# Kernel optimization log

Measured on AMD Instinct MI355X. Metric: run time of the kernel, lower is better.

## Reference

```python
import jax, jax.numpy as jnp
import numpy as np

S, B, V, E, H, T = 256, 32, 50000, 300, 256, 32  # seq, batch, vocab, emb, lstm hidden, num_tags


def _lstm_dir(x, w_ih, w_hh, b_ih, b_hh, reverse):
    # x: [S, B, in]; gates in PyTorch order i, f, g, o
    Bm, Hm = x.shape[1], w_hh.shape[1]
    def step(carry, xt):
        h, c = carry
        g = xt @ w_ih.T + b_ih + h @ w_hh.T + b_hh  # [B, 4H]
        i, f, gg, o = jnp.split(g, 4, axis=-1)
        c = jax.nn.sigmoid(f) * c + jax.nn.sigmoid(i) * jnp.tanh(gg)
        h = jax.nn.sigmoid(o) * jnp.tanh(c)
        return (h, c), h
    init = (jnp.zeros((Bm, Hm), x.dtype), jnp.zeros((Bm, Hm), x.dtype))
    _, hs = jax.lax.scan(step, init, x, reverse=reverse)
    return hs  # [S, B, H]


def _crf_loss(em, tags, start, trans, end):
    # em: [S, B, T]; torchcrf log-likelihood, reduction='sum', full mask
    bidx = jnp.arange(em.shape[1])
    # numerator (gold path score)
    emit = jnp.take_along_axis(em, tags[:, :, None], axis=2)[..., 0].sum(0)  # [B]
    tr = trans[tags[:-1], tags[1:]].sum(0)  # [B]
    num = start[tags[0]] + emit + tr + end[tags[-1]]
    # denominator (forward algorithm)
    def step(alpha, e):
        alpha = jax.nn.logsumexp(alpha[:, :, None] + trans[None] + e[:, None, :], axis=1)
        return alpha, None
    alpha0 = start[None] + em[0]  # [B, T]
    alpha, _ = jax.lax.scan(step, alpha0, em[1:])
    logZ = jax.nn.logsumexp(alpha + end[None], axis=-1)  # [B]
    return -(num - logZ).sum()


def _viterbi(em, start, trans, end):
    def step(s, e):
        cand = s[:, :, None] + trans[None]           # [B, T_prev, T_cur]
        return cand.max(1) + e, cand.argmax(1)        # score [B,T], backptr [B,T]
    score0 = start[None] + em[0]
    score, hist = jax.lax.scan(step, score0, em[1:])  # hist: [S-1, B, T]
    last = jnp.argmax(score + end[None], axis=-1)     # [B]
    def back(tag, bp):
        prev = jnp.take_along_axis(bp, tag[:, None], axis=1)[:, 0]
        return prev, prev
    _, path_head = jax.lax.scan(back, last, hist, reverse=True)  # [S-1, B]
    return jnp.concatenate([path_head, last[None]], axis=0).astype(jnp.int32)  # [S, B]


def setup_inputs():
    key = jax.random.key(0)
    ks = jax.random.split(key, 32)
    def n(k, shape, s=0.1):
        return (jax.random.normal(k, shape, jnp.float32) * s)
    inp = {
        'words': jax.random.randint(ks[0], (S, B), 0, V),
        'chars': jax.random.randint(ks[1], (S, B, 16), 0, 100),
        'tags': jax.random.randint(ks[2], (S, B), 0, T),
        'emb_table': n(ks[3], (V, E)),
        'fc_w': n(ks[4], (T, 2 * H), float(np.sqrt(2.0 / (T + 2 * H)))),
        'fc_b': n(ks[5], (T,), float(np.sqrt(1.0 / T))),
        'crf_start': n(ks[6], (T,)),
        'crf_end': n(ks[7], (T,)),
        'crf_trans': n(ks[8], (T, T)),
    }
    i = 9
    for l, din in ((0, E), (1, 2 * H)):
        for d in ('f', 'b'):
            inp[f'w_ih_l{l}{d}'] = n(ks[i], (4 * H, din)); i += 1
            inp[f'w_hh_l{l}{d}'] = n(ks[i], (4 * H, H)); i += 1
            inp[f'b_ih_l{l}{d}'] = n(ks[i], (4 * H,)); i += 1
            inp[f'b_hh_l{l}{d}'] = n(ks[i], (4 * H,)); i += 1
    return inp


def reference(words, chars, tags, emb_table, fc_w, fc_b, crf_start, crf_end, crf_trans,
              w_ih_l0f, w_hh_l0f, b_ih_l0f, b_hh_l0f,
              w_ih_l0b, w_hh_l0b, b_ih_l0b, b_hh_l0b,
              w_ih_l1f, w_hh_l1f, b_ih_l1f, b_hh_l1f,
              w_ih_l1b, w_hh_l1b, b_ih_l1b, b_hh_l1b):
    # chars / char CNN are unused in the original forward()
    x = emb_table[words]                                   # [S, B, E]
    h0 = jnp.concatenate([
        _lstm_dir(x, w_ih_l0f, w_hh_l0f, b_ih_l0f, b_hh_l0f, False),
        _lstm_dir(x, w_ih_l0b, w_hh_l0b, b_ih_l0b, b_hh_l0b, True)], axis=-1)
    h1 = jnp.concatenate([
        _lstm_dir(h0, w_ih_l1f, w_hh_l1f, b_ih_l1f, b_hh_l1f, False),
        _lstm_dir(h0, w_ih_l1b, w_hh_l1b, b_ih_l1b, b_hh_l1b, True)], axis=-1)  # [S, B, 2H]
    em = h1 @ fc_w.T + fc_b                                # emissions [S, B, T]
    crf_out = _viterbi(em, crf_start, crf_trans, crf_end)  # [S, B] int32
    crf_loss = _crf_loss(em, tags, crf_start, crf_trans, crf_end)
    return crf_out, crf_loss
```

## Files before the change

kernel.cpp:

```cpp
#include <hip/hip_runtime.h>
#include <stdint.h>

#define S_ 256
#define B_ 32
#define H_ 256
#define G4_ 1024
#define HXW (16*132)

typedef short bf16x8 __attribute__((ext_vector_type(8)));
typedef float f32x4  __attribute__((ext_vector_type(4)));

__device__ __forceinline__ unsigned f2bf(float f){
  unsigned u = __float_as_uint(f);
  return (u + 0x7fffu + ((u >> 16) & 1u)) >> 16;
}
__device__ __forceinline__ float bfl(unsigned u){ return __uint_as_float(u << 16); }
__device__ __forceinline__ float bfh(unsigned u){ return __uint_as_float(u & 0xffff0000u); }
__device__ __forceinline__ float sigf(float x){ return 1.0f / (1.0f + __expf(-x)); }
__device__ __forceinline__ float thf(float x){
  x = fminf(fmaxf(x, -15.0f), 15.0f);
  float e = __expf(2.0f * x);
  return (e - 1.0f) / (e + 1.0f);
}

__device__ __forceinline__ int hval_ok(unsigned long long v){
  return (((unsigned)v & (unsigned)(v >> 32)) & 0x40004000u) == 0x40004000u;
}

__global__ __launch_bounds__(320) void k_prep(const int* __restrict__ words,
                                              const float* __restrict__ emb,
                                              unsigned short* __restrict__ x,
                                              unsigned* __restrict__ hbuf0){
  int row = blockIdx.x;
  int e = threadIdx.x;
  int w = words[row];
  x[row * 320 + e] = (e < 300) ? (unsigned short)f2bf(emb[w * 300 + e]) : 0;
  if (e < 256) hbuf0[row * 256 + e] = 0;
}

__global__ __launch_bounds__(256) void k_packw(
    const float* __restrict__ w0f, const float* __restrict__ w0b,
    const float* __restrict__ w1f, const float* __restrict__ w1b,
    const float* __restrict__ fw,
    unsigned short* __restrict__ wb0f, unsigned short* __restrict__ wb0b,
    unsigned short* __restrict__ wb1f, unsigned short* __restrict__ wb1b,
    unsigned short* __restrict__ fcwb){
  int r = blockIdx.x, tid = threadIdx.x;
  if (r < 2048){
    int rr = r & 1023;
    const float* src = (r < 1024) ? w0f : w0b;
    unsigned short* dst = (r < 1024) ? wb0f : wb0b;
    for (int e = tid; e < 320; e += 256)
      dst[rr * 320 + e] = (e < 300) ? (unsigned short)f2bf(src[rr * 300 + e]) : 0;
  } else if (r < 4096){
    int rr = r & 1023;
    const float* src = (r < 3072) ? w1f : w1b;
    unsigned short* dst = (r < 3072) ? wb1f : wb1b;
    for (int e = tid; e < 512; e += 256)
      dst[rr * 512 + e] = (unsigned short)f2bf(src[rr * 512 + e]);
  } else {
    int rr = r - 4096;
    for (int e = tid; e < 512; e += 256)
      fcwb[rr * 512 + e] = (unsigned short)f2bf(fw[rr * 512 + e]);
  }
}

__global__ __launch_bounds__(256) void k_gemm_bf2(
    const unsigned short* __restrict__ A, int lda, int nSteps,
    const unsigned short* __restrict__ Bf, const unsigned short* __restrict__ Bb,
    const float* __restrict__ b1f, const float* __restrict__ b2f,
    const float* __restrict__ b1b, const float* __restrict__ b2b,
    float* __restrict__ Cf, float* __restrict__ Cb){
  const int z = blockIdx.z;
  const unsigned short* __restrict__ B = z ? Bb : Bf;
  const float* __restrict__ bias1 = z ? b1b : b1f;
  const float* __restrict__ bias2 = z ? b2b : b2f;
  float* __restrict__ C = z ? Cb : Cf;

  __shared__ __align__(16) unsigned As[64 * 20];
  __shared__ __align__(16) unsigned Bs[128 * 20];
  const int tid = threadIdx.x;
  const int w = tid >> 6, lane = tid & 63;
  const int quad = lane >> 4, coln = lane & 15;
  const int m0 = blockIdx.y * 64, n0 = blockIdx.x * 128;

  f32x4 acc[8];
  #pragma unroll
  for (int i = 0; i < 8; ++i){ acc[i][0]=0.f; acc[i][1]=0.f; acc[i][2]=0.f; acc[i][3]=0.f; }

  for (int kt = 0; kt < nSteps; ++kt){
    int k0 = kt * 32;
    __syncthreads();
    {
      int row = tid >> 2, part = tid & 3;
      *(uint4*)&As[row * 20 + part * 4] =
          *(const uint4*)(A + (size_t)(m0 + row) * lda + k0 + part * 8);
    }
    #pragma unroll
    for (int i = 0; i < 2; ++i){
      int idx = tid + 256 * i;
      int row = idx >> 2, part = idx & 3;
      *(uint4*)&Bs[row * 20 + part * 4] =
          *(const uint4*)(B + (size_t)(n0 + row) * lda + k0 + part * 8);
    }
    __syncthreads();
    union { uint4 q; bf16x8 v; } au;
    au.q = *(const uint4*)&As[(w * 16 + coln) * 20 + quad * 4];
    #pragma unroll
    for (int nt = 0; nt < 8; ++nt){
      union { uint4 q; bf16x8 v; } bu;
      bu.q = *(const uint4*)&Bs[(nt * 16 + coln) * 20 + quad * 4];
      acc[nt] = __builtin_amdgcn_mfma_f32_16x16x32_bf16(au.v, bu.v, acc[nt], 0, 0, 0);
    }
  }
  #pragma unroll
  for (int nt = 0; nt < 8; ++nt){
    int col = n0 + nt * 16 + coln;
    float bs = bias1[col] + bias2[col];
    #pragma unroll
    for (int reg = 0; reg < 4; ++reg)
      C[(size_t)(m0 + w * 16 + quad * 4 + reg) * 1024 + col] = acc[nt][reg] + bs;
  }
}

__global__ __launch_bounds__(256, 1) void k_lstm2(
    const float* __restrict__ Gf, const float* __restrict__ Gb,
    const float* __restrict__ Whf, const float* __restrict__ Whb,
    unsigned* __restrict__ hbuf,
    unsigned short* __restrict__ Hout)
{
  __shared__ __align__(16) unsigned hx[2 * HXW];
  const int wg  = blockIdx.x;
  const int dir = wg >> 3, n = (wg >> 1) & 3, bh = wg & 1;
  const float* __restrict__ G  = dir ? Gb : Gf;
  const float* __restrict__ Wh = dir ? Whb : Whf;
  const int tid  = threadIdx.x;
  const int w    = tid >> 6;
  const int lane = tid & 63;
  const int quad = lane >> 4, coln = lane & 15;

  bf16x8 Wr[32];
  #pragma unroll
  for (int ks = 0; ks < 8; ++ks){
    #pragma unroll
    for (int gt = 0; gt < 4; ++gt){
      const float* wp = Wh + (size_t)(gt * 256 + (n << 6) + (w << 4) + coln) * 256
                        + ks * 32 + quad * 8;
      float4 a = *(const float4*)wp;
      float4 b = *(const float4*)(wp + 4);
      union { unsigned u[4]; bf16x8 v; } tu;
      tu.u[0] = f2bf(a.x) | (f2bf(a.y) << 16);
      tu.u[1] = f2bf(a.z) | (f2bf(a.w) << 16);
      tu.u[2] = f2bf(b.x) | (f2bf(b.y) << 16);
      tu.u[3] = f2bf(b.z) | (f2bf(b.w) << 16);
      Wr[ks * 4 + gt] = tu.v;
    }
  }

  const int gu  = (n << 6) + (w << 4) + coln;
  const int mrw = quad << 2;

  float c0 = 0.f, c1 = 0.f, c2 = 0.f, c3 = 0.f;

  for (int t = 0; t < 256; ++t){
    int s = dir ? (255 - t) : t;
    f32x4 acc[4];
    #pragma unroll
    for (int gt = 0; gt < 4; ++gt){
      const float* gp = G + (size_t)(s * 32 + bh * 16 + mrw) * 1024 + gt * 256 + gu;
      f32x4 a;
      a[0] = gp[0]; a[1] = gp[1024]; a[2] = gp[2048]; a[3] = gp[3072];
      acc[gt] = a;
    }
    unsigned* hxr = &hx[(t & 1) * HXW];
    if (t > 0){
      const unsigned* hb = hbuf + (((size_t)(t - 1) * 2 + dir) * 2 + bh) * 2048;
      int row = tid >> 4, kk = tid & 15;
      int n1 = (n + 1) & 3, n2 = (n + 2) & 3, n3 = (n + 3) & 3;
      const unsigned long long* p1 =
          (const unsigned long long*)(hb + row * 128 + n1 * 32 + kk * 2);
      const unsigned long long* p2 =
          (const unsigned long long*)(hb + row * 128 + n2 * 32 + kk * 2);
      const unsigned long long* p3 =
          (const unsigned long long*)(hb + row * 128 + n3 * 32 + kk * 2);
      unsigned long long v1, v2, v3;
      do {
        v1 = __hip_atomic_load(p1, __ATOMIC_RELAXED, __HIP_MEMORY_SCOPE_AGENT);
        v2 = __hip_atomic_load(p2, __ATOMIC_RELAXED, __HIP_MEMORY_SCOPE_AGENT);
        v3 = __hip_atomic_load(p3, __ATOMIC_RELAXED, __HIP_MEMORY_SCOPE_AGENT);
      } while (!(hval_ok(v1) && hval_ok(v2) && hval_ok(v3)));
      hxr[row * 132 + n1 * 32 + kk * 2]     = (unsigned)v1 & 0xBFFFBFFFu;
      hxr[row * 132 + n1 * 32 + kk * 2 + 1] = (unsigned)(v1 >> 32) & 0xBFFFBFFFu;
      hxr[row * 132 + n2 * 32 + kk * 2]     = (unsigned)v2 & 0xBFFFBFFFu;
      hxr[row * 132 + n2 * 32 + kk * 2 + 1] = (unsigned)(v2 >> 32) & 0xBFFFBFFFu;
      hxr[row * 132 + n3 * 32 + kk * 2]     = (unsigned)v3 & 0xBFFFBFFFu;
      hxr[row * 132 + n3 * 32 + kk * 2 + 1] = (unsigned)(v3 >> 32) & 0xBFFFBFFFu;
      __syncthreads();
      #pragma unroll
      for (int ks = 0; ks < 8; ++ks){
        union { uint4 q; bf16x8 v; } tu;
        tu.q = *(const uint4*)&hxr[coln * 132 + ks * 16 + quad * 4];
        #pragma unroll
        for (int gt = 0; gt < 4; ++gt)
          acc[gt] = __builtin_amdgcn_mfma_f32_16x16x32_bf16(tu.v, Wr[ks * 4 + gt],
                                                            acc[gt], 0, 0, 0);
      }
    }
    unsigned* hxw = &hx[((t + 1) & 1) * HXW];
    unsigned* hw  = hbuf + (((size_t)t * 2 + dir) * 2 + bh) * 2048;
    float cc[4] = {c0, c1, c2, c3};
    #pragma unroll
    for (int reg = 0; reg < 4; ++reg){
      float gi = sigf(acc[0][reg]);
      float gf = sigf(acc[1][reg]);
      float gg = thf (acc[2][reg]);
      float go = sigf(acc[3][reg]);
      float cv = gf * cc[reg] + gi * gg;
      cc[reg] = cv;
      float hv = go * thf(cv);
      unsigned hb16 = f2bf(hv);
      unsigned other = (unsigned)__shfl_xor((int)hb16, 1);
      if (!(coln & 1)){
        unsigned pair = hb16 | (other << 16);
        hxw[(mrw + reg) * 132 + (gu >> 1)] = pair;
        if (t < 255)
          __hip_atomic_store(hw + (mrw + reg) * 128 + (gu >> 1),
                             pair | 0x40004000u,
                             __ATOMIC_RELAXED, __HIP_MEMORY_SCOPE_AGENT);
      }
      Hout[(size_t)(s * 32 + bh * 16 + mrw + reg) * 512 + dir * 256 + gu] =
          (unsigned short)hb16;
    }
    c0 = cc[0]; c1 = cc[1]; c2 = cc[2]; c3 = cc[3];
  }
}

__global__ __launch_bounds__(64) void k_fc(const unsigned short* __restrict__ h1,
                                           const unsigned short* __restrict__ fw,
                                           const float* __restrict__ fb,
                                           float* __restrict__ em){
  int row = blockIdx.x;
  int lane = threadIdx.x;
  int tag = lane & 31, half = lane >> 5;
  const uint4* hp = (const uint4*)(h1 + (size_t)row * 512 + half * 256);
  const uint4* wp = (const uint4*)(fw + (size_t)tag * 512 + half * 256);
  float acc = 0.0f;
  #pragma unroll 8
  for (int i = 0; i < 32; ++i){
    uint4 h = hp[i], v = wp[i];
    acc += bfl(h.x) * bfl(v.x) + bfh(h.x) * bfh(v.x)
         + bfl(h.y) * bfl(v.y) + bfh(h.y) * bfh(v.y)
         + bfl(h.z) * bfl(v.z) + bfh(h.z) * bfh(v.z)
         + bfl(h.w) * bfl(v.w) + bfh(h.w) * bfh(v.w);
  }
  acc += __shfl_down(acc, 32);
  if (half == 0) em[row * 32 + tag] = acc + fb[tag];
}

__global__ __launch_bounds__(64) void k_crf(const float* __restrict__ em,
                                            const int* __restrict__ tags,
                                            const float* __restrict__ start,
                                            const float* __restrict__ trans,
                                            const float* __restrict__ endv,
                                            int* __restrict__ path,
                                            float* __restrict__ lossb){
  __shared__ float tr[1024];
  __shared__ float sc[32], sc2[32];
  __shared__ unsigned char bp[255][32];
  int b = blockIdx.x & 31, mode = blockIdx.x >> 5;
  int t = threadIdx.x;
  for (int i = t; i < 1024; i += 64) tr[i] = trans[i];
  if (t < 32) sc[t] = start[t] + em[b * 32 + t];
  __syncthreads();
  if (mode == 0){
    for (int s = 1; s < 256; ++s){
      if (t < 32){
        float best = -1e30f; int bi = 0;
        for (int p = 0; p < 32; ++p){
          float v = sc[p] + tr[p * 32 + t];
          if (v > best){ best = v; bi = p; }
        }
        sc2[t] = best + em[(s * 32 + b) * 32 + t];
        bp[s - 1][t] = (unsigned char)bi;
      }
      __syncthreads();
      if (t < 32) sc[t] = sc2[t];
      __syncthreads();
    }
    if (t == 0){
      float best = -1e30f; int bi = 0;
      for (int p = 0; p < 32; ++p){
        float v = sc[p] + endv[p];
        if (v > best){ best = v; bi = p; }
      }
      int cur = bi;
      path[255 * 32 + b] = cur;
      for (int s = 254; s >= 0; --s){
        cur = bp[s][cur];
        path[s * 32 + b] = cur;
      }
    }
  } else {
    for (int s = 1; s < 256; ++s){
      if (t < 32){
        float m = -1e30f;
        for (int p = 0; p < 32; ++p){ float v = sc[p] + tr[p * 32 + t]; m = fmaxf(m, v); }
        float ss = 0.0f;
        for (int p = 0; p < 32; ++p){ ss += __expf(sc[p] + tr[p * 32 + t] - m); }
        sc2[t] = m + __logf(ss) + em[(s * 32 + b) * 32 + t];
      }
      __syncthreads();
      if (t < 32) sc[t] = sc2[t];
      __syncthreads();
    }
    float nsum = 0.0f;
    for (int s = t; s < 256; s += 64){
      int tg = tags[s * 32 + b];
      nsum += em[(s * 32 + b) * 32 + tg];
      if (s == 0) nsum += start[tg];
      else        nsum += tr[tags[(s - 1) * 32 + b] * 32 + tg];
      if (s == 255) nsum += endv[tg];
    }
    #pragma unroll
    for (int off = 32; off >= 1; off >>= 1) nsum += __shfl_down(nsum, off);
    if (t == 0){
      float m = -1e30f;
      for (int p = 0; p < 32; ++p) m = fmaxf(m, sc[p] + endv[p]);
      float ss = 0.0f;
      for (int p = 0; p < 32; ++p) ss += __expf(sc[p] + endv[p] - m);
      lossb[b] = m + __logf(ss) - nsum;
    }
  }
}

__global__ __launch_bounds__(64) void k_final(const float* __restrict__ lossb,
                                              float* __restrict__ outp){
  float v = (threadIdx.x < 32) ? lossb[threadIdx.x] : 0.0f;
  #pragma unroll
  for (int off = 32; off >= 1; off >>= 1) v += __shfl_down(v, off);
  if (threadIdx.x == 0) outp[0] = v;
}

extern "C" void kernel_launch(void* const* d_in, const int* in_sizes, int n_in,
                              void* d_out, int out_size, void* d_ws, size_t ws_size,
                              hipStream_t stream){
  const int*   words  = (const int*)d_in[0];
  const int*   tags   = (const int*)d_in[2];
  const float* emb    = (const float*)d_in[3];
  const float* fcw    = (const float*)d_in[4];
  const float* fcb    = (const float*)d_in[5];
  const float* cstart = (const float*)d_in[6];
  const float* cend   = (const float*)d_in[7];
  const float* ctrans = (const float*)d_in[8];
  const float* w_ih[4] = {(const float*)d_in[9],  (const float*)d_in[13],
                          (const float*)d_in[17], (const float*)d_in[21]};
  const float* w_hh[4] = {(const float*)d_in[10], (const float*)d_in[14],
                          (const float*)d_in[18], (const float*)d_in[22]};
  const float* b_ih[4] = {(const float*)d_in[11], (const float*)d_in[15],
                          (const float*)d_in[19], (const float*)d_in[23]};
  const float* b_hh[4] = {(const float*)d_in[12], (const float*)d_in[16],
                          (const float*)d_in[20], (const float*)d_in[24]};

  char* base = (char*)d_ws;
  unsigned short* x    = (unsigned short*)base;
  float* Gf            = (float*)(base + 5242880);
  float* Gb            = (float*)(base + 38797312);
  unsigned short* h0   = (unsigned short*)(base + 72351744);
  unsigned short* h1   = (unsigned short*)(base + 80740352);
  unsigned short* wb0f = (unsigned short*)(base + 89128960);
  unsigned short* wb0b = (unsigned short*)(base + 89784320);
  unsigned short* wb1f = (unsigned short*)(base + 90439680);
  unsigned short* wb1b = (unsigned short*)(base + 91488256);
  unsigned short* fcwb = (unsigned short*)(base + 92536832);
  float* lossb         = (float*)(base + 92569600);
  float* em            = Gf;
  unsigned* hbuf0 = (unsigned*)h1;
  unsigned* hbuf1 = (unsigned*)h0;

  k_prep<<<8192, 320, 0, stream>>>(words, emb, x, hbuf0);
  k_packw<<<4128, 256, 0, stream>>>(w_ih[0], w_ih[1], w_ih[2], w_ih[3], fcw,
                                    wb0f, wb0b, wb1f, wb1b, fcwb);

  k_gemm_bf2<<<dim3(8, 128, 2), 256, 0, stream>>>(x, 320, 10, wb0f, wb0b,
                                                  b_ih[0], b_hh[0], b_ih[1], b_hh[1],
                                                  Gf, Gb);
  k_lstm2<<<16, 256, 0, stream>>>(Gf, Gb, w_hh[0], w_hh[1], hbuf0, h0);

  k_gemm_bf2<<<dim3(8, 128, 2), 256, 0, stream>>>(h0, 512, 16, wb1f, wb1b,
                                                  b_ih[2], b_hh[2], b_ih[3], b_hh[3],
                                                  Gf, Gb);
  k_lstm2<<<16, 256, 0, stream>>>(Gf, Gb, w_hh[2], w_hh[3], hbuf1, h1);

  k_fc<<<8192, 64, 0, stream>>>(h1, fcwb, fcb, em);

  k_crf<<<64, 64, 0, stream>>>(em, tags, cstart, ctrans, cend, (int*)d_out, lossb);
  k_final<<<1, 64, 0, stream>>>(lossb, ((float*)d_out) + (out_size - 1));
}
```

Measured before the change: 1.505 ms.

## Duplicate LSTM hidden-state exchange buffers and drop CRF block barriers

The LSTM recurrent kernel now publishes each hidden-state chunk to two buffers: one through a volatile store and one through an agent-scope atomic. Consumers poll the first with inline-asm sc0 loads and fall back to the second, aiming to cut cross-workgroup exchange latency on each of the 256 steps. The CRF kernel keeps its transition column in registers and replaces the per-step double __syncthreads with a single-wavefront LDS exchange using s_waitcnt. This adds four zero-fill streams in prep and leans on memory-ordering assumptions: sc0 loads plus volatile stores, and no barrier inside a 64-thread block, which may be fragile.

```diff
diff --git a/kernel.cpp b/kernel.cpp
--- a/kernel.cpp
+++ b/kernel.cpp
@@ -30,12 +30,18 @@
 __global__ __launch_bounds__(320) void k_prep(const int* __restrict__ words,
                                               const float* __restrict__ emb,
                                               unsigned short* __restrict__ x,
-                                              unsigned* __restrict__ hbuf0){
+                                              unsigned* __restrict__ zA0,
+                                              unsigned* __restrict__ zB0,
+                                              unsigned* __restrict__ zA1,
+                                              unsigned* __restrict__ zB1){
   int row = blockIdx.x;
   int e = threadIdx.x;
   int w = words[row];
   x[row * 320 + e] = (e < 300) ? (unsigned short)f2bf(emb[w * 300 + e]) : 0;
-  if (e < 256) hbuf0[row * 256 + e] = 0;
+  if (e < 256){
+    int i = row * 256 + e;
+    zA0[i] = 0; zB0[i] = 0; zA1[i] = 0; zB1[i] = 0;
+  }
 }
 
 __global__ __launch_bounds__(256) void k_packw(
@@ -126,7 +132,7 @@
 __global__ __launch_bounds__(256, 1) void k_lstm2(
     const float* __restrict__ Gf, const float* __restrict__ Gb,
     const float* __restrict__ Whf, const float* __restrict__ Whb,
-    unsigned* __restrict__ hbuf,
+    unsigned* __restrict__ hbufA, unsigned* __restrict__ hbufB,
     unsigned short* __restrict__ Hout)
 {
   __shared__ __align__(16) unsigned hx[2 * HXW];
@@ -174,27 +180,56 @@
     }
     unsigned* hxr = &hx[(t & 1) * HXW];
     if (t > 0){
-      const unsigned* hb = hbuf + (((size_t)(t - 1) * 2 + dir) * 2 + bh) * 2048;
+      size_t off = (((size_t)(t - 1) * 2 + dir) * 2 + bh) * 2048;
+      const unsigned* hbA = hbufA + off;
+      const unsigned* hbB = hbufB + off;
       int row = tid >> 4, kk = tid & 15;
       int n1 = (n + 1) & 3, n2 = (n + 2) & 3, n3 = (n + 3) & 3;
-      const unsigned long long* p1 =
-          (const unsigned long long*)(hb + row * 128 + n1 * 32 + kk * 2);
-      const unsigned long long* p2 =
-          (const unsigned long long*)(hb + row * 128 + n2 * 32 + kk * 2);
-      const unsigned long long* p3 =
-          (const unsigned long long*)(hb + row * 128 + n3 * 32 + kk * 2);
-      unsigned long long v1, v2, v3;
+      int b1 = row * 128 + n1 * 32 + kk * 2;
+      int b2 = row * 128 + n2 * 32 + kk * 2;
+      int b3 = row * 128 + n3 * 32 + kk * 2;
+      const unsigned* pA1 = hbA + b1;
+      const unsigned* pA2 = hbA + b2;
+      const unsigned* pA3 = hbA + b3;
+      unsigned long long r1 = 0, r2 = 0, r3 = 0;
+      bool d1 = false, d2 = false, d3 = false;
       do {
-        v1 = __hip_atomic_load(p1, __ATOMIC_RELAXED, __HIP_MEMORY_SCOPE_AGENT);
-        v2 = __hip_atomic_load(p2, __ATOMIC_RELAXED, __HIP_MEMORY_SCOPE_AGENT);
-        v3 = __hip_atomic_load(p3, __ATOMIC_RELAXED, __HIP_MEMORY_SCOPE_AGENT);
-      } while (!(hval_ok(v1) && hval_ok(v2) && hval_ok(v3)));
-      hxr[row * 132 + n1 * 32 + kk * 2]     = (unsigned)v1 & 0xBFFFBFFFu;
-      hxr[row * 132 + n1 * 32 + kk * 2 + 1] = (unsigned)(v1 >> 32) & 0xBFFFBFFFu;
-      hxr[row * 132 + n2 * 32 + kk * 2]     = (unsigned)v2 & 0xBFFFBFFFu;
-      hxr[row * 132 + n2 * 32 + kk * 2 + 1] = (unsigned)(v2 >> 32) & 0xBFFFBFFFu;
-      hxr[row * 132 + n3 * 32 + kk * 2]     = (unsigned)v3 & 0xBFFFBFFFu;
-      hxr[row * 132 + n3 * 32 + kk * 2 + 1] = (unsigned)(v3 >> 32) & 0xBFFFBFFFu;
+        unsigned long long a1, a2, a3;
+        asm volatile("global_load_dwordx2 %0, %3, off sc0\n\t"
+                     "global_load_dwordx2 %1, %4, off sc0\n\t"
+                     "global_load_dwordx2 %2, %5, off sc0\n\t"
+                     "s_waitcnt vmcnt(0)"
+                     : "=&v"(a1), "=&v"(a2), "=&v"(a3)
+                     : "v"(pA1), "v"(pA2), "v"(pA3) : "memory");
+        if (!d1 && hval_ok(a1)){ r1 = a1; d1 = true; }
+        if (!d2 && hval_ok(a2)){ r2 = a2; d2 = true; }
+        if (!d3 && hval_ok(a3)){ r3 = a3; d3 = true; }
+        if (d1 && d2 && d3) break;
+        if (!d1){
+          unsigned long long v = __hip_atomic_load(
+              (const unsigned long long*)(hbB + b1),
+              __ATOMIC_RELAXED, __HIP_MEMORY_SCOPE_AGENT);
+          if (hval_ok(v)){ r1 = v; d1 = true; }
+        }
+        if (!d2){
+          unsigned long long v = __hip_atomic_load(
+              (const unsigned long long*)(hbB + b2),
+              __ATOMIC_RELAXED, __HIP_MEMORY_SCOPE_AGENT);
+          if (hval_ok(v)){ r2 = v; d2 = true; }
+        }
+        if (!d3){
+          unsigned long long v = __hip_atomic_load(
+              (const unsigned long long*)(hbB + b3),
+              __ATOMIC_RELAXED, __HIP_MEMORY_SCOPE_AGENT);
+          if (hval_ok(v)){ r3 = v; d3 = true; }
+        }
+      } while (!(d1 && d2 && d3));
+      hxr[row * 132 + n1 * 32 + kk * 2]     = (unsigned)r1 & 0xBFFFBFFFu;
+      hxr[row * 132 + n1 * 32 + kk * 2 + 1] = (unsigned)(r1 >> 32) & 0xBFFFBFFFu;
+      hxr[row * 132 + n2 * 32 + kk * 2]     = (unsigned)r2 & 0xBFFFBFFFu;
+      hxr[row * 132 + n2 * 32 + kk * 2 + 1] = (unsigned)(r2 >> 32) & 0xBFFFBFFFu;
+      hxr[row * 132 + n3 * 32 + kk * 2]     = (unsigned)r3 & 0xBFFFBFFFu;
+      hxr[row * 132 + n3 * 32 + kk * 2 + 1] = (unsigned)(r3 >> 32) & 0xBFFFBFFFu;
       __syncthreads();
       #pragma unroll
       for (int ks = 0; ks < 8; ++ks){
@@ -207,7 +242,9 @@
       }
     }
     unsigned* hxw = &hx[((t + 1) & 1) * HXW];
-    unsigned* hw  = hbuf + (((size_t)t * 2 + dir) * 2 + bh) * 2048;
+    size_t woff = (((size_t)t * 2 + dir) * 2 + bh) * 2048;
+    unsigned* hwA = hbufA + woff;
+    unsigned* hwB = hbufB + woff;
     float cc[4] = {c0, c1, c2, c3};
     #pragma unroll
     for (int reg = 0; reg < 4; ++reg){
@@ -223,10 +260,13 @@
       if (!(coln & 1)){
         unsigned pair = hb16 | (other << 16);
         hxw[(mrw + reg) * 132 + (gu >> 1)] = pair;
-        if (t < 255)
-          __hip_atomic_store(hw + (mrw + reg) * 128 + (gu >> 1),
-                             pair | 0x40004000u,
+        if (t < 255){
+          unsigned enc = pair | 0x40004000u;
+          int idx = (mrw + reg) * 128 + (gu >> 1);
+          ((volatile unsigned*)hwA)[idx] = enc;
+          __hip_atomic_store(hwB + idx, enc,
                              __ATOMIC_RELAXED, __HIP_MEMORY_SCOPE_AGENT);
+        }
       }
       Hout[(size_t)(s * 32 + bh * 16 + mrw + reg) * 512 + dir * 256 + gu] =
           (unsigned short)hb16;
@@ -264,33 +304,35 @@
                                             const float* __restrict__ endv,
                                             int* __restrict__ path,
                                             float* __restrict__ lossb){
-  __shared__ float tr[1024];
-  __shared__ float sc[32], sc2[32];
+  __shared__ float al[32];
   __shared__ unsigned char bp[255][32];
   int b = blockIdx.x & 31, mode = blockIdx.x >> 5;
   int t = threadIdx.x;
-  for (int i = t; i < 1024; i += 64) tr[i] = trans[i];
-  if (t < 32) sc[t] = start[t] + em[b * 32 + t];
-  __syncthreads();
+  int tg = t & 31;
+  float tr_reg[32];
+  #pragma unroll
+  for (int p = 0; p < 32; ++p) tr_reg[p] = trans[p * 32 + tg];
+  float a = start[tg] + em[b * 32 + tg];
   if (mode == 0){
     for (int s = 1; s < 256; ++s){
+      if (t < 32) al[t] = a;
+      __builtin_amdgcn_s_waitcnt(0);
+      float best = -1e30f; int bi = 0;
+      for (int p = 0; p < 32; ++p){
+        float v = al[p] + tr_reg[p];
+        if (v > best){ best = v; bi = p; }
+      }
       if (t < 32){
-        float best = -1e30f; int bi = 0;
-        for (int p = 0; p < 32; ++p){
-          float v = sc[p] + tr[p * 32 + t];
-          if (v > best){ best = v; bi = p; }
-        }
-        sc2[t] = best + em[(s * 32 + b) * 32 + t];
+        a = best + em[(s * 32 + b) * 32 + t];
         bp[s - 1][t] = (unsigned char)bi;
       }
-      __syncthreads();
-      if (t < 32) sc[t] = sc2[t];
-      __syncthreads();
-    }
+    }
+    if (t < 32) al[t] = a;
+    __builtin_amdgcn_s_waitcnt(0);
     if (t == 0){
       float best = -1e30f; int bi = 0;
       for (int p = 0; p < 32; ++p){
-        float v = sc[p] + endv[p];
+        float v = al[p] + endv[p];
         if (v > best){ best = v; bi = p; }
       }
       int cur = bi;
@@ -302,32 +344,35 @@
     }
   } else {
     for (int s = 1; s < 256; ++s){
-      if (t < 32){
-        float m = -1e30f;
-        for (int p = 0; p < 32; ++p){ float v = sc[p] + tr[p * 32 + t]; m = fmaxf(m, v); }
-        float ss = 0.0f;
-        for (int p = 0; p < 32; ++p){ ss += __expf(sc[p] + tr[p * 32 + t] - m); }
-        sc2[t] = m + __logf(ss) + em[(s * 32 + b) * 32 + t];
-      }
-      __syncthreads();
-      if (t < 32) sc[t] = sc2[t];
-      __syncthreads();
-    }
+      if (t < 32) al[t] = a;
+      __builtin_amdgcn_s_waitcnt(0);
+      float m = -1e30f;
+      for (int p = 0; p < 32; ++p){
+        float v = al[p] + tr_reg[p];
+        m = fmaxf(m, v);
+      }
+      float ss = 0.0f;
+      for (int p = 0; p < 32; ++p)
+        ss += __expf(al[p] + tr_reg[p] - m);
+      if (t < 32) a = m + __logf(ss) + em[(s * 32 + b) * 32 + t];
+    }
+    if (t < 32) al[t] = a;
+    __builtin_amdgcn_s_waitcnt(0);
     float nsum = 0.0f;
     for (int s = t; s < 256; s += 64){
-      int tg = tags[s * 32 + b];
-      nsum += em[(s * 32 + b) * 32 + tg];
-      if (s == 0) nsum += start[tg];
-      else        nsum += tr[tags[(s - 1) * 32 + b] * 32 + tg];
-      if (s == 255) nsum += endv[tg];
+      int tgd = tags[s * 32 + b];
+      nsum += em[(s * 32 + b) * 32 + tgd];
+      if (s == 0) nsum += start[tgd];
+      else        nsum += trans[tags[(s - 1) * 32 + b] * 32 + tgd];
+      if (s == 255) nsum += endv[tgd];
     }
     #pragma unroll
     for (int off = 32; off >= 1; off >>= 1) nsum += __shfl_down(nsum, off);
     if (t == 0){
       float m = -1e30f;
-      for (int p = 0; p < 32; ++p) m = fmaxf(m, sc[p] + endv[p]);
+      for (int p = 0; p < 32; ++p) m = fmaxf(m, al[p] + endv[p]);
       float ss = 0.0f;
-      for (int p = 0; p < 32; ++p) ss += __expf(sc[p] + endv[p] - m);
+      for (int p = 0; p < 32; ++p) ss += __expf(al[p] + endv[p] - m);
       lossb[b] = m + __logf(ss) - nsum;
     }
   }
@@ -373,23 +418,25 @@
   unsigned short* wb1b = (unsigned short*)(base + 91488256);
   unsigned short* fcwb = (unsigned short*)(base + 92536832);
   float* lossb         = (float*)(base + 92569600);
+  unsigned* hbufB0     = (unsigned*)(base + 92569728);
+  unsigned* hbufB1     = (unsigned*)(base + 100958336);
   float* em            = Gf;
-  unsigned* hbuf0 = (unsigned*)h1;
-  unsigned* hbuf1 = (unsigned*)h0;
-
-  k_prep<<<8192, 320, 0, stream>>>(words, emb, x, hbuf0);
+  unsigned* hbufA0 = (unsigned*)h1;
+  unsigned* hbufA1 = (unsigned*)h0;
+
+  k_prep<<<8192, 320, 0, stream>>>(words, emb, x, hbufA0, hbufB0, hbufA1, hbufB1);
   k_packw<<<4128, 256, 0, stream>>>(w_ih[0], w_ih[1], w_ih[2], w_ih[3], fcw,
                                     wb0f, wb0b, wb1f, wb1b, fcwb);
 
   k_gemm_bf2<<<dim3(8, 128, 2), 256, 0, stream>>>(x, 320, 10, wb0f, wb0b,
                                                   b_ih[0], b_hh[0], b_ih[1], b_hh[1],
                                                   Gf, Gb);
-  k_lstm2<<<16, 256, 0, stream>>>(Gf, Gb, w_hh[0], w_hh[1], hbuf0, h0);
+  k_lstm2<<<16, 256, 0, stream>>>(Gf, Gb, w_hh[0], w_hh[1], hbufA0, hbufB0, h0);
 
   k_gemm_bf2<<<dim3(8, 128, 2), 256, 0, stream>>>(h0, 512, 16, wb1f, wb1b,
                                                   b_ih[2], b_hh[2], b_ih[3], b_hh[3],
                                                   Gf, Gb);
-  k_lstm2<<<16, 256, 0, stream>>>(Gf, Gb, w_hh[2], w_hh[3], hbuf1, h1);
+  k_lstm2<<<16, 256, 0, stream>>>(Gf, Gb, w_hh[2], w_hh[3], hbufA1, hbufB1, h1);
 
   k_fc<<<8192, 64, 0, stream>>>(h1, fcwb, fcb, em);
 
```

Measured after the change: 2.245 ms. 49.2% more time.
